# Performance work log

Hardware: AMD Instinct MI355X
Metric: run time of the kernel (lower is better)

## Reference

```python
import jax, jax.numpy as jnp
import numpy as np

DIM, H, DH = 1024, 16, 64
SCALE = 1.0 / np.sqrt(DH)


def setup_inputs() -> dict:
    key = jax.random.key(0)
    ks = jax.random.split(key, 16)
    B, S = 2, 2048
    glorot = jax.nn.initializers.glorot_uniform()
    def qkv(k):
        return glorot(k, (DIM, H, DH), jnp.float32)
    inp = {
        "x": jax.random.normal(ks[0], (B, S, DIM), jnp.float32),
        "layer_idx": 3,
        "lambda_param": jnp.full((1,), 0.8, jnp.float32),
    }
    for i, br in enumerate(["1", "2"]):
        base = 1 + i * 4
        inp[f"Wq{br}"] = qkv(ks[base])
        inp[f"Wk{br}"] = qkv(ks[base + 1])
        inp[f"Wv{br}"] = qkv(ks[base + 2])
        inp[f"Wo{br}"] = glorot(ks[base + 3], (H, DH, DIM), jnp.float32).reshape(H, DH, DIM)
        inp[f"bq{br}"] = jnp.zeros((H, DH), jnp.float32)
        inp[f"bk{br}"] = jnp.zeros((H, DH), jnp.float32)
        inp[f"bv{br}"] = jnp.zeros((H, DH), jnp.float32)
        inp[f"bo{br}"] = jnp.zeros((DIM,), jnp.float32)
    inp["Wp"] = glorot(ks[9], (DIM, DIM), jnp.float32)
    inp["bp"] = jnp.zeros((DIM,), jnp.float32)
    return inp


def _mha(x, Wq, bq, Wk, bk, Wv, bv, Wo, bo):
    # x: [B,S,D]; per-head projections as in keras.layers.MultiHeadAttention
    q = jnp.einsum("bsd,dhk->bshk", x, Wq) + bq   # [B,S,H,Dh]
    k = jnp.einsum("bsd,dhk->bshk", x, Wk) + bk
    v = jnp.einsum("bsd,dhk->bshk", x, Wv) + bv
    scores = jnp.einsum("bqhd,bkhd->bhqk", q, k) * SCALE  # [B,H,S,S]
    attn = jax.nn.softmax(scores, axis=-1)
    o = jnp.einsum("bhqk,bkhd->bqhd", attn, v)            # [B,S,H,Dh]
    return jnp.einsum("bqhd,hdo->bqo", o, Wo) + bo        # [B,S,D]


def _get_lambda(lambda_param, layer_idx):
    lf = jnp.asarray(layer_idx, jnp.float32)
    exp_term = jnp.exp(-0.3 * jnp.maximum(lf - 1.0, 0.0))
    init = 0.8 - 0.6 * exp_term
    return jnp.clip(init * lambda_param[0], 0.1, 0.9)


def reference(x, layer_idx, lambda_param,
              Wq1, bq1, Wk1, bk1, Wv1, bv1, Wo1, bo1,
              Wq2, bq2, Wk2, bk2, Wv2, bv2, Wo2, bo2,
              Wp, bp):
    a1 = _mha(x, Wq1, bq1, Wk1, bk1, Wv1, bv1, Wo1, bo1)
    a2 = _mha(x, Wq2, bq2, Wk2, bk2, Wv2, bv2, Wo2, bo2)
    lam = _get_lambda(lambda_param, layer_idx)
    diff = a1 - lam * a2
    return diff @ Wp + bp  # dropout is identity at inference
```

## Files before the change

### kernel.cpp

```cpp
#include <hip/hip_runtime.h>
#include <math.h>

typedef unsigned short u16;
typedef __attribute__((ext_vector_type(8))) short bf16x8;
typedef __attribute__((ext_vector_type(4))) float f32x4;
typedef __attribute__((ext_vector_type(4))) unsigned short u16x4;
typedef __attribute__((ext_vector_type(8))) unsigned short u16x8;

constexpr int Sq = 2048, Dm = 1024, Hh = 16, DH = 64;
constexpr int NT = 4096;
constexpr float SEXP = 0.125f * 1.44269504f;

__device__ __forceinline__ u16 f2bf(float f) {
    unsigned u = __float_as_uint(f);
    return (u16)((u + 0x7FFF + ((u >> 16) & 1)) >> 16);
}

__device__ __forceinline__ void async16(u16* lds, const u16* g) {
    __builtin_amdgcn_global_load_lds(
        (const __attribute__((address_space(1))) unsigned int*)g,
        (__attribute__((address_space(3))) unsigned int*)lds, 16, 0, 0);
}

__device__ __forceinline__ float lam_of(const int* lidx, const float* lamp) {
    float lf = (float)lidx[0];
    float init = 0.8f - 0.6f * __expf(-0.3f * fmaxf(lf - 1.0f, 0.0f));
    return fminf(fmaxf(init * lamp[0], 0.1f), 0.9f);
}

__device__ __forceinline__ void gemm_tile_128(
    const u16* __restrict__ A, const u16* __restrict__ Bt, int K,
    int aRow0, int bCol0, u16* As, u16* Bs, f32x4 acc[4][4])
{
    const int tid = threadIdx.x;
    const int w = tid >> 6, lane = tid & 63;
    const int ln = lane & 15, quad = lane >> 4;
    const int wm = (w >> 1) * 64, wn = (w & 1) * 64;
    const int l3 = lane & 7, lr8 = lane >> 3;

    for (int kt = 0; kt < K; kt += 64) {
        __syncthreads();
        #pragma unroll
        for (int c0 = 0; c0 < 4; ++c0) {
            int c = w * 4 + c0;
            int lr = c * 8 + lr8;
            int sc = l3 ^ (lr & 7);
            async16(As + c * 512, A + (size_t)(aRow0 + lr) * K + kt + sc * 8);
            async16(Bs + c * 512, Bt + (size_t)(bCol0 + lr) * K + kt + sc * 8);
        }
        __syncthreads();
        #pragma unroll
        for (int kc = 0; kc < 2; ++kc) {
            bf16x8 af[4], bfr[4];
            #pragma unroll
            for (int mt = 0; mt < 4; ++mt)
                af[mt] = *(const bf16x8*)(As + (wm + mt * 16 + ln) * 64 +
                                          (((kc * 4 + quad) ^ (ln & 7)) * 8));
            #pragma unroll
            for (int nt = 0; nt < 4; ++nt)
                bfr[nt] = *(const bf16x8*)(Bs + (wn + nt * 16 + ln) * 64 +
                                           (((kc * 4 + quad) ^ (ln & 7)) * 8));
            #pragma unroll
            for (int mt = 0; mt < 4; ++mt)
                #pragma unroll
                for (int nt = 0; nt < 4; ++nt)
                    acc[mt][nt] = __builtin_amdgcn_mfma_f32_16x16x32_bf16(
                        af[mt], bfr[nt], acc[mt][nt], 0, 0, 0);
        }
    }
}

__device__ __forceinline__ void gemm_tile_64(
    const u16* __restrict__ A, const u16* __restrict__ Bt, int K,
    int aRow0, int bCol0, u16* As, u16* Bs, f32x4 acc[2][4])
{
    const int tid = threadIdx.x;
    const int w = tid >> 6, lane = tid & 63;
    const int ln = lane & 15, quad = lane >> 4;
    const int wm = (w >> 1) * 32, wn = (w & 1) * 64;
    const int l3 = lane & 7, lr8 = lane >> 3;

    for (int kt = 0; kt < K; kt += 64) {
        __syncthreads();
        #pragma unroll
        for (int c0 = 0; c0 < 2; ++c0) {
            int c = w * 2 + c0;
            int lr = c * 8 + lr8;
            int sc = l3 ^ (lr & 7);
            async16(As + c * 512, A + (size_t)(aRow0 + lr) * K + kt + sc * 8);
        }
        #pragma unroll
        for (int c0 = 0; c0 < 4; ++c0) {
            int c = w * 4 + c0;
            int lr = c * 8 + lr8;
            int sc = l3 ^ (lr & 7);
            async16(Bs + c * 512, Bt + (size_t)(bCol0 + lr) * K + kt + sc * 8);
        }
        __syncthreads();
        #pragma unroll
        for (int kc = 0; kc < 2; ++kc) {
            bf16x8 af[2], bfr[4];
            #pragma unroll
            for (int mt = 0; mt < 2; ++mt)
                af[mt] = *(const bf16x8*)(As + (wm + mt * 16 + ln) * 64 +
                                          (((kc * 4 + quad) ^ (ln & 7)) * 8));
            #pragma unroll
            for (int nt = 0; nt < 4; ++nt)
                bfr[nt] = *(const bf16x8*)(Bs + (wn + nt * 16 + ln) * 64 +
                                           (((kc * 4 + quad) ^ (ln & 7)) * 8));
            #pragma unroll
            for (int mt = 0; mt < 2; ++mt)
                #pragma unroll
                for (int nt = 0; nt < 4; ++nt)
                    acc[mt][nt] = __builtin_amdgcn_mfma_f32_16x16x32_bf16(
                        af[mt], bfr[nt], acc[mt][nt], 0, 0, 0);
        }
    }
}

__global__ __launch_bounds__(256)
void convert_x(const float* __restrict__ x, u16* __restrict__ xb)
{
    int i = (blockIdx.x * 256 + threadIdx.x) * 4;
    float4 v = *(const float4*)(x + i);
    u16x4 o;
    o.x = f2bf(v.x); o.y = f2bf(v.y); o.z = f2bf(v.z); o.w = f2bf(v.w);
    *(u16x4*)(xb + i) = o;
}

struct TcP { const float* src[9]; u16* dst[9]; int ld[9]; int coff[9]; };

__global__ __launch_bounds__(256)
void wconv(TcP p, const int* __restrict__ lidx, const float* __restrict__ lamp)
{
    __shared__ float t[64][65];
    const int z = blockIdx.z;
    const float scale = (z == 7) ? -lam_of(lidx, lamp) : 1.0f;
    const float* __restrict__ src = p.src[z];
    u16* __restrict__ dst = p.dst[z];
    const int kb = blockIdx.y * 64, nb = blockIdx.x * 64;
    const int tid = threadIdx.x;
    {
        int r = tid >> 2, cs = (tid & 3) * 16;
        #pragma unroll
        for (int j4 = 0; j4 < 16; j4 += 4) {
            float4 v = *(const float4*)&src[(size_t)(kb + r) * 1024 + nb + cs + j4];
            t[r][cs + j4 + 0] = v.x; t[r][cs + j4 + 1] = v.y;
            t[r][cs + j4 + 2] = v.z; t[r][cs + j4 + 3] = v.w;
        }
    }
    __syncthreads();
    {
        int n = tid >> 2, ks = (tid & 3) * 16;
        u16x8 a, b;
        #pragma unroll
        for (int j = 0; j < 8; ++j) a[j] = f2bf(scale * t[ks + j][n]);
        #pragma unroll
        for (int j = 0; j < 8; ++j) b[j] = f2bf(scale * t[ks + 8 + j][n]);
        u16* o = &dst[(size_t)(nb + n) * p.ld[z] + p.coff[z] + kb + ks];
        *(u16x8*)o = a;
        *(u16x8*)(o + 8) = b;
    }
}

struct QkvP { const u16* Wt[6]; const float* bias[6]; u16* out[6]; };

__global__ __launch_bounds__(256, 3)
void qkv_mfma(const u16* __restrict__ xb, QkvP p)
{
    __shared__ u16 As[128 * 64], Bs[128 * 64];
    const int z = blockIdx.z;
    const int type = (z < 3) ? z : z - 3;
    const int aRow0 = blockIdx.y * 128, nCol0 = blockIdx.x * 128;
    f32x4 acc[4][4] = {};
    gemm_tile_128(xb, p.Wt[z], 1024, aRow0, nCol0, As, Bs, acc);

    const float* __restrict__ bias = p.bias[z];
    u16* __restrict__ out = p.out[z];
    const int tid = threadIdx.x, w = tid >> 6, lane = tid & 63;
    const int ln = lane & 15, quad = lane >> 4;
    const int wm = (w >> 1) * 64, wn = (w & 1) * 64;
    #pragma unroll
    for (int mt = 0; mt < 4; ++mt) {
        #pragma unroll
        for (int nt = 0; nt < 4; ++nt) {
            int gn = nCol0 + wn + nt * 16 + ln;
            int h = gn >> 6, dh = gn & 63;
            float bv = bias[gn];
            #pragma unroll
            for (int r = 0; r < 4; ++r) {
                int gm = aRow0 + wm + mt * 16 + quad * 4 + r;
                int b = gm >> 11, s = gm & (Sq - 1);
                size_t bh = (size_t)(b * Hh + h);
                u16 val = f2bf(acc[mt][nt][r] + bv);
                size_t idx;
                if (type == 0) {
                    idx = bh * 131072 + (size_t)s * 64 + dh;
                } else if (type == 1) {
                    idx = bh * 131072 + (size_t)(s >> 5) * 2048 +
                          (size_t)((dh >> 5) * 2 + ((s >> 4) & 1)) * 512 +
                          (size_t)(((dh >> 3) & 3) * 16 + (s & 15)) * 8 + (dh & 7);
                } else {
                    int kidx = ((s & 15) * 2) + ((s >> 4) & 1);
                    idx = bh * 131072 + (size_t)(s >> 5) * 2048 +
                          (size_t)(dh >> 4) * 512 +
                          (size_t)((kidx >> 3) * 16 + (dh & 15)) * 8 + (kidx & 7);
                }
                out[idx] = val;
            }
        }
    }
}

__global__ __launch_bounds__(256, 2)
void attn_mfma(const u16* __restrict__ q1, const u16* __restrict__ kf1,
               const u16* __restrict__ vf1,
               const u16* __restrict__ q2, const u16* __restrict__ kf2,
               const u16* __restrict__ vf2, u16* __restrict__ ocat)
{
    __shared__ __align__(16) char smem[3 * 17408 + 768];

    const int qblk = blockIdx.x, bh = blockIdx.y, br = blockIdx.z;
    const u16* __restrict__ q  = br ? q2  : q1;
    const u16* __restrict__ kf = br ? kf2 : kf1;
    const u16* __restrict__ vf = br ? vf2 : vf1;

    const int tid = threadIdx.x, w = tid >> 6, lane = tid & 63;
    const int ln = lane & 15, quad = lane >> 4;
    char* Pbase = smem + w * 5120;

    const u16* qbase = q + (size_t)bh * 131072 + (size_t)(qblk * 64) * 64;
    bf16x8 qf[4][2];
    #pragma unroll
    for (int mt = 0; mt < 4; ++mt)
        #pragma unroll
        for (int kc = 0; kc < 2; ++kc)
            qf[mt][kc] = *(const bf16x8*)(qbase + (mt * 16 + ln) * 64 +
                                          kc * 32 + quad * 8);

    bf16x8 ones;
    #pragma unroll
    for (int j = 0; j < 8; ++j) ones[j] = (short)0x3F80;

    f32x4 oacc[4][4] = {};
    f32x4 lacc[4] = {};

    const u16* kbase = kf + (size_t)bh * 131072 + lane * 8;
    const u16* vbase = vf + (size_t)bh * 131072 + lane * 8;

    for (int it = 0; it < 16; ++it) {
        const int kt = it * 4 + w;
        const u16* kp = kbase + (size_t)kt * 2048;
        const u16* vp = vbase + (size_t)kt * 2048;

        bf16x8 kfr[2][2], vfr[4];
        #pragma unroll
        for (int kc = 0; kc < 2; ++kc)
            #pragma unroll
            for (int nt = 0; nt < 2; ++nt)
                kfr[nt][kc] = *(const bf16x8*)(kp + (kc * 2 + nt) * 512);
        #pragma unroll
        for (int dt = 0; dt < 4; ++dt)
            vfr[dt] = *(const bf16x8*)(vp + dt * 512);

        f32x4 sacc[4][2] = {};
        #pragma unroll
        for (int kc = 0; kc < 2; ++kc)
            #pragma unroll
            for (int mt = 0; mt < 4; ++mt)
                #pragma unroll
                for (int nt = 0; nt < 2; ++nt)
                    sacc[mt][nt] = __builtin_amdgcn_mfma_f32_16x16x32_bf16(
                        qf[mt][kc], kfr[nt][kc], sacc[mt][nt], 0, 0, 0);

        #pragma unroll
        for (int mt = 0; mt < 4; ++mt) {
            #pragma unroll
            for (int r = 0; r < 4; ++r) {
                float p0 = exp2f(sacc[mt][0][r] * SEXP);
                float p1 = exp2f(sacc[mt][1][r] * SEXP);
                unsigned a  = __float_as_uint(p0) + 0x8000u;
                unsigned b2 = __float_as_uint(p1) + 0x8000u;
                unsigned pk = __builtin_amdgcn_perm(b2, a, 0x07060302);
                int row = mt * 16 + quad * 4 + r;
                *(unsigned*)(Pbase + row * 80 + (((ln >> 2) ^ r) << 4) +
                             ((ln & 3) << 2)) = pk;
            }
        }

        #pragma unroll
        for (int mt = 0; mt < 4; ++mt) {
            bf16x8 pf = *(const bf16x8*)(Pbase + (mt * 16 + ln) * 80 +
                                         ((quad ^ (ln & 3)) << 4));
            lacc[mt] = __builtin_amdgcn_mfma_f32_16x16x32_bf16(
                pf, ones, lacc[mt], 0, 0, 0);
            #pragma unroll
            for (int dt = 0; dt < 4; ++dt)
                oacc[mt][dt] = __builtin_amdgcn_mfma_f32_16x16x32_bf16(
                    pf, vfr[dt], oacc[mt][dt], 0, 0, 0);
        }
    }

    __syncthreads();
    char* lbase = smem + 3 * 17408;
    if (w < 3) {
        char* ob = smem + w * 17408;
        #pragma unroll
        for (int mt = 0; mt < 4; ++mt) {
            #pragma unroll
            for (int dt = 0; dt < 4; ++dt)
                #pragma unroll
                for (int r = 0; r < 4; ++r)
                    *(float*)(ob + (mt * 16 + quad * 4 + r) * 272 +
                              (dt * 16 + ln) * 4) = oacc[mt][dt][r];
            if (ln == 0)
                #pragma unroll
                for (int r = 0; r < 4; ++r)
                    *(float*)(lbase + w * 256 + (mt * 16 + quad * 4 + r) * 4) =
                        lacc[mt][r];
        }
    }
    __syncthreads();
    if (w == 3) {
        #pragma unroll
        for (int mt = 0; mt < 4; ++mt) {
            #pragma unroll
            for (int dt = 0; dt < 4; ++dt)
                #pragma unroll
                for (int r = 0; r < 4; ++r) {
                    float* pp = (float*)(smem + (mt * 16 + quad * 4 + r) * 272 +
                                         (dt * 16 + ln) * 4);
                    *pp += oacc[mt][dt][r];
                }
            if (ln == 0)
                #pragma unroll
                for (int r = 0; r < 4; ++r) {
                    float* pp = (float*)(lbase + (mt * 16 + quad * 4 + r) * 4);
                    *pp += lacc[mt][r];
                }
        }
    }
    __syncthreads();

    {
        int qr = tid >> 2, dg = tid & 3;
        float lt = *(float*)(lbase + qr * 4) + *(float*)(lbase + 256 + qr * 4) +
                   *(float*)(lbase + 512 + qr * 4);
        float inv = 1.0f / lt;
        float vals[16];
        #pragma unroll
        for (int c = 0; c < 4; ++c) {
            f32x4 v0 = *(f32x4*)(smem + 0 * 17408 + qr * 272 + dg * 64 + c * 16);
            f32x4 v1 = *(f32x4*)(smem + 1 * 17408 + qr * 272 + dg * 64 + c * 16);
            f32x4 v2 = *(f32x4*)(smem + 2 * 17408 + qr * 272 + dg * 64 + c * 16);
            #pragma unroll
            for (int i = 0; i < 4; ++i)
                vals[c * 4 + i] = (v0[i] + v1[i] + v2[i]) * inv;
        }
        int token = (bh >> 4) * 2048 + qblk * 64 + qr;
        size_t base = (size_t)token * 2048 + br * 1024 + (bh & 15) * 64 + dg * 16;
        u16x8 o0, o1;
        #pragma unroll
        for (int i = 0; i < 8; ++i) { o0[i] = f2bf(vals[i]); o1[i] = f2bf(vals[8 + i]); }
        *(u16x8*)(ocat + base) = o0;
        *(u16x8*)(ocat + base + 8) = o1;
    }
}

__global__ __launch_bounds__(256, 4)
void combine_mfma(const u16* __restrict__ ocat, const u16* __restrict__ Wcmb,
                  const float* __restrict__ bo1, const float* __restrict__ bo2,
                  const int* __restrict__ lidx, const float* __restrict__ lamp,
                  u16* __restrict__ adiff)
{
    __shared__ u16 As[64 * 64], Bs[128 * 64];
    const int aRow0 = blockIdx.y * 64, nCol0 = blockIdx.x * 128;
    f32x4 acc[2][4] = {};
    gemm_tile_64(ocat, Wcmb, 2048, aRow0, nCol0, As, Bs, acc);

    const float lam = lam_of(lidx, lamp);
    const int tid = threadIdx.x, w = tid >> 6, lane = tid & 63;
    const int ln = lane & 15, quad = lane >> 4;
    const int wm = (w >> 1) * 32, wn = (w & 1) * 64;
    #pragma unroll
    for (int mt = 0; mt < 2; ++mt) {
        #pragma unroll
        for (int nt = 0; nt < 4; ++nt) {
            int gn = nCol0 + wn + nt * 16 + ln;
            float bv = bo1[gn] - lam * bo2[gn];
            #pragma unroll
            for (int r = 0; r < 4; ++r) {
                int gm = aRow0 + wm + mt * 16 + quad * 4 + r;
                adiff[(size_t)gm * 1024 + gn] = f2bf(acc[mt][nt][r] + bv);
            }
        }
    }
}

__global__ __launch_bounds__(256, 4)
void final_mfma(const u16* __restrict__ adiff, const u16* __restrict__ Wpt,
                const float* __restrict__ bp, float* __restrict__ outb)
{
    __shared__ u16 As[64 * 64], Bs[128 * 64];
    const int aRow0 = blockIdx.y * 64, nCol0 = blockIdx.x * 128;
    f32x4 acc[2][4] = {};
    gemm_tile_64(adiff, Wpt, 1024, aRow0, nCol0, As, Bs, acc);

    const int tid = threadIdx.x, w = tid >> 6, lane = tid & 63;
    const int ln = lane & 15, quad = lane >> 4;
    const int wm = (w >> 1) * 32, wn = (w & 1) * 64;
    #pragma unroll
    for (int mt = 0; mt < 2; ++mt) {
        #pragma unroll
        for (int nt = 0; nt < 4; ++nt) {
            int gn = nCol0 + wn + nt * 16 + ln;
            float bv = bp[gn];
            #pragma unroll
            for (int r = 0; r < 4; ++r) {
                int gm = aRow0 + wm + mt * 16 + quad * 4 + r;
                outb[(size_t)gm * 1024 + gn] = acc[mt][nt][r] + bv;
            }
        }
    }
}

extern "C" void kernel_launch(void* const* d_in, const int* in_sizes, int n_in,
                              void* d_out, int out_size, void* d_ws, size_t ws_size,
                              hipStream_t stream)
{
    const float* x    = (const float*)d_in[0];
    const int*   lidx = (const int*)  d_in[1];
    const float* lamp = (const float*)d_in[2];
    const float* Wq1  = (const float*)d_in[3];
    const float* Wk1  = (const float*)d_in[4];
    const float* Wv1  = (const float*)d_in[5];
    const float* Wo1  = (const float*)d_in[6];
    const float* bq1  = (const float*)d_in[7];
    const float* bk1  = (const float*)d_in[8];
    const float* bv1  = (const float*)d_in[9];
    const float* bo1  = (const float*)d_in[10];
    const float* Wq2  = (const float*)d_in[11];
    const float* Wk2  = (const float*)d_in[12];
    const float* Wv2  = (const float*)d_in[13];
    const float* Wo2  = (const float*)d_in[14];
    const float* bq2  = (const float*)d_in[15];
    const float* bk2  = (const float*)d_in[16];
    const float* bv2  = (const float*)d_in[17];
    const float* bo2  = (const float*)d_in[18];
    const float* Wp   = (const float*)d_in[19];
    const float* bp   = (const float*)d_in[20];

    char* wsb = (char*)d_ws;
    const size_t MB = 1 << 20;
    u16* xb   = (u16*)(wsb + 0 * MB);
    u16* Wt0  = (u16*)(wsb + 8 * MB);
    u16* Wcmb = (u16*)(wsb + 20 * MB);
    u16* Wpt  = (u16*)(wsb + 24 * MB);
    u16* qb1  = (u16*)(wsb + 26 * MB);
    u16* kb1  = (u16*)(wsb + 34 * MB);
    u16* vb1  = (u16*)(wsb + 42 * MB);
    u16* qb2  = (u16*)(wsb + 50 * MB);
    u16* kb2  = (u16*)(wsb + 58 * MB);
    u16* vb2  = (u16*)(wsb + 66 * MB);
    u16* ocat = (u16*)(wsb + 74 * MB);
    u16* adif = (u16*)(wsb + 90 * MB);

    convert_x<<<dim3(NT * Dm / 1024), dim3(256), 0, stream>>>(x, xb);

    TcP tp;
    const float* wsrc[9] = {Wq1, Wk1, Wv1, Wq2, Wk2, Wv2, Wo1, Wo2, Wp};
    for (int i = 0; i < 9; ++i) tp.src[i] = wsrc[i];
    for (int i = 0; i < 6; ++i) { tp.dst[i] = Wt0 + (size_t)i * 1024 * 1024; tp.ld[i] = 1024; tp.coff[i] = 0; }
    tp.dst[6] = Wcmb; tp.ld[6] = 2048; tp.coff[6] = 0;
    tp.dst[7] = Wcmb; tp.ld[7] = 2048; tp.coff[7] = 1024;
    tp.dst[8] = Wpt;  tp.ld[8] = 1024; tp.coff[8] = 0;
    wconv<<<dim3(16, 16, 9), dim3(256), 0, stream>>>(tp, lidx, lamp);

    QkvP qp;
    qp.Wt[0] = Wt0 + 0 * 1048576; qp.bias[0] = bq1; qp.out[0] = qb1;
    qp.Wt[1] = Wt0 + 1 * 1048576; qp.bias[1] = bk1; qp.out[1] = kb1;
    qp.Wt[2] = Wt0 + 2 * 1048576; qp.bias[2] = bv1; qp.out[2] = vb1;
    qp.Wt[3] = Wt0 + 3 * 1048576; qp.bias[3] = bq2; qp.out[3] = qb2;
    qp.Wt[4] = Wt0 + 4 * 1048576; qp.bias[4] = bk2; qp.out[4] = kb2;
    qp.Wt[5] = Wt0 + 5 * 1048576; qp.bias[5] = bv2; qp.out[5] = vb2;
    qkv_mfma<<<dim3(8, 32, 6), dim3(256), 0, stream>>>(xb, qp);

    attn_mfma<<<dim3(32, 32, 2), dim3(256), 0, stream>>>(
        qb1, kb1, vb1, qb2, kb2, vb2, ocat);

    combine_mfma<<<dim3(8, 64), dim3(256), 0, stream>>>(
        ocat, Wcmb, bo1, bo2, lidx, lamp, adif);

    final_mfma<<<dim3(8, 64), dim3(256), 0, stream>>>(
        adif, Wpt, bp, (float*)d_out);
}
```

Before: 377.3 us.

## Fold softmax scale into Q projection and shrink attention LDS via atomic merge

The Q projection epilogue now multiplies by the softmax scale times log2(e), so the attention kernel can call exp2 directly on the raw scores. The attention kernel's four-wave partial-output merge now zero-initialises one buffer and accumulates into it with LDS atomicAdd, where it previously used three separate partial buffers. This cuts shared memory from about 53 KB to 20 KB, and launch bounds are raised to 4 blocks per CU. The grid is reordered so the batch-head index varies fastest. Risks include register pressure from the higher occupancy target, contention on the LDS atomics, and a small change in rounding because Q is scaled before the bf16 cast.

```diff
diff --git a/kernel.cpp b/kernel.cpp
--- a/kernel.cpp
+++ b/kernel.cpp
@@ -192,15 +192,19 @@
                 int gm = aRow0 + wm + mt * 16 + quad * 4 + r;
                 int b = gm >> 11, s = gm & (Sq - 1);
                 size_t bh = (size_t)(b * Hh + h);
-                u16 val = f2bf(acc[mt][nt][r] + bv);
+                float fv = acc[mt][nt][r] + bv;
                 size_t idx;
+                u16 val;
                 if (type == 0) {
+                    val = f2bf(fv * SEXP);
                     idx = bh * 131072 + (size_t)s * 64 + dh;
                 } else if (type == 1) {
+                    val = f2bf(fv);
                     idx = bh * 131072 + (size_t)(s >> 5) * 2048 +
                           (size_t)((dh >> 5) * 2 + ((s >> 4) & 1)) * 512 +
                           (size_t)(((dh >> 3) & 3) * 16 + (s & 15)) * 8 + (dh & 7);
                 } else {
+                    val = f2bf(fv);
                     int kidx = ((s & 15) * 2) + ((s >> 4) & 1);
                     idx = bh * 131072 + (size_t)(s >> 5) * 2048 +
                           (size_t)(dh >> 4) * 512 +
@@ -212,15 +216,15 @@
     }
 }
 
-__global__ __launch_bounds__(256, 2)
+__global__ __launch_bounds__(256, 4)
 void attn_mfma(const u16* __restrict__ q1, const u16* __restrict__ kf1,
                const u16* __restrict__ vf1,
                const u16* __restrict__ q2, const u16* __restrict__ kf2,
                const u16* __restrict__ vf2, u16* __restrict__ ocat)
 {
-    __shared__ __align__(16) char smem[3 * 17408 + 768];
-
-    const int qblk = blockIdx.x, bh = blockIdx.y, br = blockIdx.z;
+    __shared__ __align__(16) char smem[20480];
+
+    const int bh = blockIdx.x, qblk = blockIdx.y, br = blockIdx.z;
     const u16* __restrict__ q  = br ? q2  : q1;
     const u16* __restrict__ kf = br ? kf2 : kf1;
     const u16* __restrict__ vf = br ? vf2 : vf1;
@@ -277,8 +281,8 @@
         for (int mt = 0; mt < 4; ++mt) {
             #pragma unroll
             for (int r = 0; r < 4; ++r) {
-                float p0 = exp2f(sacc[mt][0][r] * SEXP);
-                float p1 = exp2f(sacc[mt][1][r] * SEXP);
+                float p0 = exp2f(sacc[mt][0][r]);
+                float p1 = exp2f(sacc[mt][1][r]);
                 unsigned a  = __float_as_uint(p0) + 0x8000u;
                 unsigned b2 = __float_as_uint(p1) + 0x8000u;
                 unsigned pk = __builtin_amdgcn_perm(b2, a, 0x07060302);
@@ -302,60 +306,34 @@
     }
 
     __syncthreads();
-    char* lbase = smem + 3 * 17408;
-    if (w < 3) {
-        char* ob = smem + w * 17408;
-        #pragma unroll
-        for (int mt = 0; mt < 4; ++mt) {
-            #pragma unroll
-            for (int dt = 0; dt < 4; ++dt)
-                #pragma unroll
-                for (int r = 0; r < 4; ++r)
-                    *(float*)(ob + (mt * 16 + quad * 4 + r) * 272 +
-                              (dt * 16 + ln) * 4) = oacc[mt][dt][r];
-            if (ln == 0)
-                #pragma unroll
-                for (int r = 0; r < 4; ++r)
-                    *(float*)(lbase + w * 256 + (mt * 16 + quad * 4 + r) * 4) =
-                        lacc[mt][r];
-        }
-    }
+    float* mrg  = (float*)smem;
+    float* lmrg = (float*)(smem + 17408);
+    for (int i = tid; i < 4416; i += 256) ((float*)smem)[i] = 0.0f;
     __syncthreads();
-    if (w == 3) {
-        #pragma unroll
-        for (int mt = 0; mt < 4; ++mt) {
-            #pragma unroll
-            for (int dt = 0; dt < 4; ++dt)
-                #pragma unroll
-                for (int r = 0; r < 4; ++r) {
-                    float* pp = (float*)(smem + (mt * 16 + quad * 4 + r) * 272 +
-                                         (dt * 16 + ln) * 4);
-                    *pp += oacc[mt][dt][r];
-                }
-            if (ln == 0)
-                #pragma unroll
-                for (int r = 0; r < 4; ++r) {
-                    float* pp = (float*)(lbase + (mt * 16 + quad * 4 + r) * 4);
-                    *pp += lacc[mt][r];
-                }
-        }
+    #pragma unroll
+    for (int mt = 0; mt < 4; ++mt) {
+        #pragma unroll
+        for (int dt = 0; dt < 4; ++dt)
+            #pragma unroll
+            for (int r = 0; r < 4; ++r)
+                atomicAdd(&mrg[(mt * 16 + quad * 4 + r) * 68 + dt * 16 + ln],
+                          oacc[mt][dt][r]);
+        if (ln == 0)
+            #pragma unroll
+            for (int r = 0; r < 4; ++r)
+                atomicAdd(&lmrg[mt * 16 + quad * 4 + r], lacc[mt][r]);
     }
     __syncthreads();
 
     {
         int qr = tid >> 2, dg = tid & 3;
-        float lt = *(float*)(lbase + qr * 4) + *(float*)(lbase + 256 + qr * 4) +
-                   *(float*)(lbase + 512 + qr * 4);
-        float inv = 1.0f / lt;
+        float inv = 1.0f / lmrg[qr];
         float vals[16];
         #pragma unroll
         for (int c = 0; c < 4; ++c) {
-            f32x4 v0 = *(f32x4*)(smem + 0 * 17408 + qr * 272 + dg * 64 + c * 16);
-            f32x4 v1 = *(f32x4*)(smem + 1 * 17408 + qr * 272 + dg * 64 + c * 16);
-            f32x4 v2 = *(f32x4*)(smem + 2 * 17408 + qr * 272 + dg * 64 + c * 16);
-            #pragma unroll
-            for (int i = 0; i < 4; ++i)
-                vals[c * 4 + i] = (v0[i] + v1[i] + v2[i]) * inv;
+            f32x4 v0 = *(f32x4*)(mrg + qr * 68 + dg * 16 + c * 4);
+            #pragma unroll
+            for (int i = 0; i < 4; ++i) vals[c * 4 + i] = v0[i] * inv;
         }
         int token = (bh >> 4) * 2048 + qblk * 64 + qr;
         size_t base = (size_t)token * 2048 + br * 1024 + (bh & 15) * 64 + dg * 16;
```

After: 1.073 ms. 184% more time.
